# Kernel tuning notes

Measured on AMD Instinct MI355X. Metric: run time of the kernel, lower is better.

The kernel has to match this reference:

```python
import jax, jax.numpy as jnp
import numpy as np

R, K, H_IN, W_IN = 512, 17, 56, 56   # rois, keypoints, heatmap size
ROI_H = ROI_W = 96                   # = ceil(BOX_LEN), fixed by construction
BOX_LEN = 95.5                       # all boxes have this side length
A = -0.75                            # PyTorch bicubic coefficient


def _cubic(x):
    x = jnp.abs(x)
    near = ((A + 2.0) * x - (A + 3.0)) * x * x + 1.0
    far = A * (((x - 5.0) * x + 8.0) * x - 4.0)
    return jnp.where(x <= 1.0, near, jnp.where(x < 2.0, far, 0.0))


def _resize_matrix(out_size, in_size):
    """Dense [out,in] bicubic interpolation matrix (align_corners=False, border-replicate)."""
    scale = in_size / out_size
    src = (jnp.arange(out_size, dtype=jnp.float32) + 0.5) * scale - 0.5
    base = jnp.floor(src).astype(jnp.int32)
    taps = base[:, None] + jnp.arange(-1, 3)                      # [out, 4]
    w = _cubic(src[:, None] - taps.astype(jnp.float32))           # weights from unclamped dist
    taps = jnp.clip(taps, 0, in_size - 1)                         # replicate border
    rows = jnp.broadcast_to(jnp.arange(out_size)[:, None], taps.shape)
    return jnp.zeros((out_size, in_size), jnp.float32).at[rows, taps].add(w)


def setup_inputs() -> dict:
    key = jax.random.key(0)
    k1, k2 = jax.random.split(key)
    masks = jax.random.normal(k1, (R, K, H_IN, W_IN), dtype=jnp.float32)
    offs = jax.random.uniform(k2, (R, 2), jnp.float32, 0.0, 400.0)
    # corner format (c0_start, c1_start, c0_end, c1_end); all lengths == BOX_LEN
    boxes = jnp.concatenate([offs, offs + BOX_LEN], axis=1)
    return {"masks": masks, "boxes": boxes}


def reference(masks, boxes):
    My = _resize_matrix(ROI_H, H_IN)   # [ROI_H, H_IN]
    Mx = _resize_matrix(ROI_W, W_IN)   # [ROI_W, W_IN]
    # separable bicubic resize of every ROI heatmap: [R,K,ROI_H,ROI_W]
    roi = jnp.einsum('hi,rkij,wj->rkhw', My, masks, Mx)
    flat = roi.reshape(R, K, ROI_H * ROI_W)
    pos = jnp.argmax(flat, axis=-1)                                # [R,K]
    y = pos // ROI_W
    x = pos % ROI_W
    scores = jnp.take_along_axis(flat, pos[..., None], axis=-1)[..., 0]  # logit at argmax
    len0 = jnp.maximum(boxes[:, 2] - boxes[:, 0], 1.0)
    len1 = jnp.maximum(boxes[:, 3] - boxes[:, 1], 1.0)
    corr0 = (len0 / ROI_H)[:, None]
    corr1 = (len1 / ROI_W)[:, None]
    p0 = (y.astype(jnp.float32) + 0.5) * corr0 + boxes[:, 0:1]
    p1 = (x.astype(jnp.float32) + 0.5) * corr1 + boxes[:, 1:2]
    predictions = jnp.stack([p0, p1, jnp.ones_like(p0)], axis=1)   # [R, n_dim+1, K]
    return predictions, scores
```

## Files before the change

### kernel.cpp

```cpp
#include <hip/hip_runtime.h>

#define R_    512
#define K_    17
#define HIN   56
#define WIN   56
#define OUTS  96
#define NMAP  (R_ * K_)
#define NT    384
#define RST   98
#define TROWS 60

typedef float v2f __attribute__((ext_vector_type(2)));

constexpr float cubic_c(float xin) {
    float x = xin < 0.0f ? -xin : xin;
    const float A = -0.75f;
    if (x <= 1.0f) return ((A + 2.0f) * x - (A + 3.0f)) * x * x + 1.0f;
    if (x < 2.0f)  return A * (((x - 5.0f) * x + 8.0f) * x - 4.0f);
    return 0.0f;
}

struct XTabT {
    float w[OUTS][4];
    int   s[OUTS];
    constexpr XTabT() : w{}, s{} {
        for (int o = 0; o < OUTS; ++o) {
            float src = ((float)o + 0.5f) * (56.0f / 96.0f) - 0.5f;
            int base = (int)src;
            if ((float)base > src) --base;
            int st = base - 1;
            if (st < 0) st = 0;
            if (st > HIN - 4) st = HIN - 4;
            s[o] = st;
            for (int q = 0; q < 4; ++q) {
                int tap = base - 1 + q;
                float wt = cubic_c(src - (float)tap);
                int p = tap < 0 ? 0 : (tap > HIN - 1 ? HIN - 1 : tap);
                w[o][p - st] += wt;
            }
        }
    }
};
constexpr XTabT XT;

struct YTabT {
    float w[12][4];
    int   d[12];
    constexpr YTabT() : w{}, d{} {
        for (int ph = 0; ph < 12; ++ph) {
            float src = ((float)ph + 0.5f) * (56.0f / 96.0f) - 0.5f;
            int base = (int)src;
            if ((float)base > src) --base;
            d[ph] = base - 1;
            for (int q = 0; q < 4; ++q)
                w[ph][q] = cubic_c(src - (float)(base - 1 + q));
        }
    }
};
constexpr YTabT YT;

template<int G>
__device__ __forceinline__ void p1_cols(const float* __restrict__ r0,
                                        const float* __restrict__ r1,
                                        v2f* __restrict__ dst) {
    constexpr int FS = (G == 0) ? 0 : (G == 1) ? 2 : (G == 2) ? 4
                     : (G == 3) ? 6 : (G == 4) ? 9 : 11;
    constexpr int NF = (G == 2 || G == 3) ? 4 : 3;
    v2f rr[NF * 4];
    const float4* A = (const float4*)r0 + FS;
    const float4* B = (const float4*)r1 + FS;
#pragma unroll
    for (int i = 0; i < NF; ++i) {
        float4 a = A[i], b = B[i];
        rr[4 * i + 0] = (v2f){a.x, b.x};
        rr[4 * i + 1] = (v2f){a.y, b.y};
        rr[4 * i + 2] = (v2f){a.z, b.z};
        rr[4 * i + 3] = (v2f){a.w, b.w};
    }
#pragma unroll
    for (int i = 0; i < 8; ++i) {
        const int o0 = 16 * G + 2 * i, o1 = o0 + 1;
        const int s0 = XT.s[o0] - 4 * FS, s1 = XT.s[o1] - 4 * FS;
        v2f a0 = rr[s0] * (v2f){XT.w[o0][0], XT.w[o0][0]};
        a0 = __builtin_elementwise_fma((v2f){XT.w[o0][1], XT.w[o0][1]}, rr[s0 + 1], a0);
        a0 = __builtin_elementwise_fma((v2f){XT.w[o0][2], XT.w[o0][2]}, rr[s0 + 2], a0);
        a0 = __builtin_elementwise_fma((v2f){XT.w[o0][3], XT.w[o0][3]}, rr[s0 + 3], a0);
        v2f a1 = rr[s1] * (v2f){XT.w[o1][0], XT.w[o1][0]};
        a1 = __builtin_elementwise_fma((v2f){XT.w[o1][1], XT.w[o1][1]}, rr[s1 + 1], a1);
        a1 = __builtin_elementwise_fma((v2f){XT.w[o1][2], XT.w[o1][2]}, rr[s1 + 2], a1);
        a1 = __builtin_elementwise_fma((v2f){XT.w[o1][3], XT.w[o1][3]}, rr[s1 + 3], a1);
        float4 st = {a0.x, a0.y, a1.x, a1.y};
        *(float4*)(dst + 2 * i) = st;
    }
}

__device__ __forceinline__ v2f yv(const v2f* __restrict__ c, int hh) {
    const int ph = hh % 12, bb = hh / 12;
    const int i0 = 7 * bb + YT.d[ph] + 2;
    v2f acc = c[i0] * (v2f){YT.w[ph][0], YT.w[ph][0]};
    acc = __builtin_elementwise_fma((v2f){YT.w[ph][1], YT.w[ph][1]}, c[i0 + 1], acc);
    acc = __builtin_elementwise_fma((v2f){YT.w[ph][2], YT.w[ph][2]}, c[i0 + 2], acc);
    acc = __builtin_elementwise_fma((v2f){YT.w[ph][3], YT.w[ph][3]}, c[i0 + 3], acc);
    return acc;
}

__global__ __launch_bounds__(NT)
void _Keypointer_kernel(const float* __restrict__ masks,
                        const float* __restrict__ boxes,
                        float* __restrict__ out) {
    __shared__ __align__(16) v2f tmp[TROWS * RST];
    __shared__ v2f wmax[6];
    __shared__ int candp[2];

    const int t   = threadIdx.x;
    const int bm0 = 2 * blockIdx.x;
    const int g   = t >> 6;
    const int w   = t & 63;

    const int srcrow = min(max(w - 2, 0), HIN - 1);
    const int phys   = min(w, TROWS - 1);
    const float* r0 = masks + (size_t)bm0 * (HIN * WIN) + srcrow * WIN;
    const float* r1 = r0 + HIN * WIN;
    v2f* dst = tmp + phys * RST + 16 * g;
    if      (g == 0) p1_cols<0>(r0, r1, dst);
    else if (g == 1) p1_cols<1>(r0, r1, dst);
    else if (g == 2) p1_cols<2>(r0, r1, dst);
    else if (g == 3) p1_cols<3>(r0, r1, dst);
    else if (g == 4) p1_cols<4>(r0, r1, dst);
    else             p1_cols<5>(r0, r1, dst);

    if (t == 0) { candp[0] = 0x7fffffff; candp[1] = 0x7fffffff; }
    __syncthreads();

    const int q    = t / 96;
    const int col  = t - 96 * q;
    const int h0   = 24 * q;
    const v2f* cb  = tmp + (14 * q) * RST + col;
    v2f c[18];
#pragma unroll
    for (int i = 0; i < 18; ++i) c[i] = cb[i * RST];

    v2f vmax = {-INFINITY, -INFINITY};
#pragma unroll
    for (int hh = 0; hh < 24; ++hh)
        vmax = __builtin_elementwise_max(vmax, yv(c, hh));

    float m0 = vmax.x, m1 = vmax.y;
#pragma unroll
    for (int off = 32; off > 0; off >>= 1) {
        m0 = fmaxf(m0, __shfl_down(m0, off, 64));
        m1 = fmaxf(m1, __shfl_down(m1, off, 64));
    }
    if (w == 0) wmax[g] = (v2f){m0, m1};
    __syncthreads();

    const float M0 = fmaxf(fmaxf(fmaxf(wmax[0].x, wmax[1].x), fmaxf(wmax[2].x, wmax[3].x)),
                           fmaxf(wmax[4].x, wmax[5].x));
    const float M1 = fmaxf(fmaxf(fmaxf(wmax[0].y, wmax[1].y), fmaxf(wmax[2].y, wmax[3].y)),
                           fmaxf(wmax[4].y, wmax[5].y));

    if (vmax.x == M0 || vmax.y == M1) {
        int c0 = 0x7fffffff, c1 = 0x7fffffff;
#pragma unroll
        for (int hh = 0; hh < 24; ++hh) {
            v2f a = yv(c, hh);
            int fp = (h0 + hh) * OUTS + col;
            if (a.x == M0) c0 = min(c0, fp);
            if (a.y == M1) c1 = min(c1, fp);
        }
        if (c0 != 0x7fffffff) atomicMin(&candp[0], c0);
        if (c1 != 0x7fffffff) atomicMin(&candp[1], c1);
    }
    __syncthreads();

    if (t < 2) {
        const int map = bm0 + t;
        const float M = t ? M1 : M0;
        const int bp  = candp[t];
        const int r = map / K_, k = map - r * K_;
        const int y = bp / OUTS, x = bp - y * OUTS;
        const float b0f = boxes[r * 4 + 0], b1f = boxes[r * 4 + 1];
        const float b2f = boxes[r * 4 + 2], b3f = boxes[r * 4 + 3];
        const float corr0 = fmaxf(b2f - b0f, 1.0f) / (float)OUTS;
        const float corr1 = fmaxf(b3f - b1f, 1.0f) / (float)OUTS;
        const float p0 = ((float)y + 0.5f) * corr0 + b0f;
        const float p1 = ((float)x + 0.5f) * corr1 + b1f;
        out[(r * 3 + 0) * K_ + k] = p0;
        out[(r * 3 + 1) * K_ + k] = p1;
        out[(r * 3 + 2) * K_ + k] = 1.0f;
        out[R_ * 3 * K_ + r * K_ + k] = M;
    }
}

extern "C" void kernel_launch(void* const* d_in, const int* in_sizes, int n_in,
                              void* d_out, int out_size, void* d_ws, size_t ws_size,
                              hipStream_t stream) {
    const float* masks = (const float*)d_in[0];
    const float* boxes = (const float*)d_in[1];
    float* out = (float*)d_out;
    _Keypointer_kernel<<<NMAP / 2, NT, 0, stream>>>(masks, boxes, out);
}
```

Measured before the change: 159.3 us.

## Make kernel persistent with register prefetch of next map pair

Launches a fixed grid where each block processes several map pairs in a loop. It prefetches the next pair's mask rows into registers while computing the current pair's horizontal pass and reduction. This is meant to hide global load latency and reduce per-block launch overhead, at the cost of extra registers and an additional barrier per iteration.

After: 242.1 us. +51.9%, slower.

```diff
diff --git a/kernel.cpp b/kernel.cpp
--- a/kernel.cpp
+++ b/kernel.cpp
@@ -7,6 +7,8 @@
 #define OUTS  96
 #define NMAP  (R_ * K_)
 #define NT    384
+#define GRID  1088
+#define ITERS 4
 #define RST   98
 #define TROWS 60
 
@@ -59,23 +61,35 @@
 };
 constexpr YTabT YT;
 
+template<int G> struct P1G {
+    static constexpr int FS = (G == 0) ? 0 : (G == 1) ? 2 : (G == 2) ? 4
+                            : (G == 3) ? 6 : (G == 4) ? 9 : 11;
+    static constexpr int NF = (G == 2 || G == 3) ? 4 : 3;
+};
+
 template<int G>
-__device__ __forceinline__ void p1_cols(const float* __restrict__ r0,
+__device__ __forceinline__ void p1_load(const float* __restrict__ r0,
                                         const float* __restrict__ r1,
+                                        float4* __restrict__ pa,
+                                        float4* __restrict__ pb) {
+    const float4* A = (const float4*)r0 + P1G<G>::FS;
+    const float4* B = (const float4*)r1 + P1G<G>::FS;
+#pragma unroll
+    for (int i = 0; i < P1G<G>::NF; ++i) { pa[i] = A[i]; pb[i] = B[i]; }
+}
+
+template<int G>
+__device__ __forceinline__ void p1_comp(const float4* __restrict__ pa,
+                                        const float4* __restrict__ pb,
                                         v2f* __restrict__ dst) {
-    constexpr int FS = (G == 0) ? 0 : (G == 1) ? 2 : (G == 2) ? 4
-                     : (G == 3) ? 6 : (G == 4) ? 9 : 11;
-    constexpr int NF = (G == 2 || G == 3) ? 4 : 3;
+    constexpr int FS = P1G<G>::FS, NF = P1G<G>::NF;
     v2f rr[NF * 4];
-    const float4* A = (const float4*)r0 + FS;
-    const float4* B = (const float4*)r1 + FS;
 #pragma unroll
     for (int i = 0; i < NF; ++i) {
-        float4 a = A[i], b = B[i];
-        rr[4 * i + 0] = (v2f){a.x, b.x};
-        rr[4 * i + 1] = (v2f){a.y, b.y};
-        rr[4 * i + 2] = (v2f){a.z, b.z};
-        rr[4 * i + 3] = (v2f){a.w, b.w};
+        rr[4 * i + 0] = (v2f){pa[i].x, pb[i].x};
+        rr[4 * i + 1] = (v2f){pa[i].y, pb[i].y};
+        rr[4 * i + 2] = (v2f){pa[i].z, pb[i].z};
+        rr[4 * i + 3] = (v2f){pa[i].w, pb[i].w};
     }
 #pragma unroll
     for (int i = 0; i < 8; ++i) {
@@ -94,6 +108,25 @@
     }
 }
 
+__device__ __forceinline__ void do_load(int g, const float* r0, const float* r1,
+                                        float4* pa, float4* pb) {
+    if      (g == 0) p1_load<0>(r0, r1, pa, pb);
+    else if (g == 1) p1_load<1>(r0, r1, pa, pb);
+    else if (g == 2) p1_load<2>(r0, r1, pa, pb);
+    else if (g == 3) p1_load<3>(r0, r1, pa, pb);
+    else if (g == 4) p1_load<4>(r0, r1, pa, pb);
+    else             p1_load<5>(r0, r1, pa, pb);
+}
+
+__device__ __forceinline__ void do_comp(int g, const float4* pa, const float4* pb, v2f* dst) {
+    if      (g == 0) p1_comp<0>(pa, pb, dst);
+    else if (g == 1) p1_comp<1>(pa, pb, dst);
+    else if (g == 2) p1_comp<2>(pa, pb, dst);
+    else if (g == 3) p1_comp<3>(pa, pb, dst);
+    else if (g == 4) p1_comp<4>(pa, pb, dst);
+    else             p1_comp<5>(pa, pb, dst);
+}
+
 __device__ __forceinline__ v2f yv(const v2f* __restrict__ c, int hh) {
     const int ph = hh % 12, bb = hh / 12;
     const int i0 = 7 * bb + YT.d[ph] + 2;
@@ -113,82 +146,95 @@
     __shared__ int candp[2];
 
     const int t   = threadIdx.x;
-    const int bm0 = 2 * blockIdx.x;
     const int g   = t >> 6;
     const int w   = t & 63;
 
     const int srcrow = min(max(w - 2, 0), HIN - 1);
     const int phys   = min(w, TROWS - 1);
-    const float* r0 = masks + (size_t)bm0 * (HIN * WIN) + srcrow * WIN;
-    const float* r1 = r0 + HIN * WIN;
     v2f* dst = tmp + phys * RST + 16 * g;
-    if      (g == 0) p1_cols<0>(r0, r1, dst);
-    else if (g == 1) p1_cols<1>(r0, r1, dst);
-    else if (g == 2) p1_cols<2>(r0, r1, dst);
-    else if (g == 3) p1_cols<3>(r0, r1, dst);
-    else if (g == 4) p1_cols<4>(r0, r1, dst);
-    else             p1_cols<5>(r0, r1, dst);
-
-    if (t == 0) { candp[0] = 0x7fffffff; candp[1] = 0x7fffffff; }
-    __syncthreads();
-
-    const int q    = t / 96;
-    const int col  = t - 96 * q;
-    const int h0   = 24 * q;
-    const v2f* cb  = tmp + (14 * q) * RST + col;
-    v2f c[18];
-#pragma unroll
-    for (int i = 0; i < 18; ++i) c[i] = cb[i * RST];
-
-    v2f vmax = {-INFINITY, -INFINITY};
-#pragma unroll
-    for (int hh = 0; hh < 24; ++hh)
-        vmax = __builtin_elementwise_max(vmax, yv(c, hh));
-
-    float m0 = vmax.x, m1 = vmax.y;
-#pragma unroll
-    for (int off = 32; off > 0; off >>= 1) {
-        m0 = fmaxf(m0, __shfl_down(m0, off, 64));
-        m1 = fmaxf(m1, __shfl_down(m1, off, 64));
-    }
-    if (w == 0) wmax[g] = (v2f){m0, m1};
-    __syncthreads();
-
-    const float M0 = fmaxf(fmaxf(fmaxf(wmax[0].x, wmax[1].x), fmaxf(wmax[2].x, wmax[3].x)),
-                           fmaxf(wmax[4].x, wmax[5].x));
-    const float M1 = fmaxf(fmaxf(fmaxf(wmax[0].y, wmax[1].y), fmaxf(wmax[2].y, wmax[3].y)),
-                           fmaxf(wmax[4].y, wmax[5].y));
-
-    if (vmax.x == M0 || vmax.y == M1) {
-        int c0 = 0x7fffffff, c1 = 0x7fffffff;
-#pragma unroll
-        for (int hh = 0; hh < 24; ++hh) {
-            v2f a = yv(c, hh);
-            int fp = (h0 + hh) * OUTS + col;
-            if (a.x == M0) c0 = min(c0, fp);
-            if (a.y == M1) c1 = min(c1, fp);
-        }
-        if (c0 != 0x7fffffff) atomicMin(&candp[0], c0);
-        if (c1 != 0x7fffffff) atomicMin(&candp[1], c1);
-    }
-    __syncthreads();
-
-    if (t < 2) {
-        const int map = bm0 + t;
-        const float M = t ? M1 : M0;
-        const int bp  = candp[t];
-        const int r = map / K_, k = map - r * K_;
-        const int y = bp / OUTS, x = bp - y * OUTS;
-        const float b0f = boxes[r * 4 + 0], b1f = boxes[r * 4 + 1];
-        const float b2f = boxes[r * 4 + 2], b3f = boxes[r * 4 + 3];
-        const float corr0 = fmaxf(b2f - b0f, 1.0f) / (float)OUTS;
-        const float corr1 = fmaxf(b3f - b1f, 1.0f) / (float)OUTS;
-        const float p0 = ((float)y + 0.5f) * corr0 + b0f;
-        const float p1 = ((float)x + 0.5f) * corr1 + b1f;
-        out[(r * 3 + 0) * K_ + k] = p0;
-        out[(r * 3 + 1) * K_ + k] = p1;
-        out[(r * 3 + 2) * K_ + k] = 1.0f;
-        out[R_ * 3 * K_ + r * K_ + k] = M;
+
+    float4 pa[4], pb[4];
+
+    int pair = blockIdx.x;
+    {
+        const float* r0 = masks + (size_t)(2 * pair) * (HIN * WIN) + srcrow * WIN;
+        do_load(g, r0, r0 + HIN * WIN, pa, pb);
+    }
+
+    for (int it = 0; it < ITERS; ++it) {
+        const int bm0 = 2 * pair;
+        const int nxt = pair + GRID;
+
+        if (t == 0) { candp[0] = 0x7fffffff; candp[1] = 0x7fffffff; }
+
+        do_comp(g, pa, pb, dst);
+
+        if (it + 1 < ITERS) {
+            const float* r0 = masks + (size_t)(2 * nxt) * (HIN * WIN) + srcrow * WIN;
+            do_load(g, r0, r0 + HIN * WIN, pa, pb);
+        }
+        __syncthreads();
+
+        const int q    = t / 96;
+        const int col  = t - 96 * q;
+        const int h0   = 24 * q;
+        const v2f* cb  = tmp + (14 * q) * RST + col;
+        v2f c[18];
+#pragma unroll
+        for (int i = 0; i < 18; ++i) c[i] = cb[i * RST];
+
+        v2f vmax = {-INFINITY, -INFINITY};
+#pragma unroll
+        for (int hh = 0; hh < 24; ++hh)
+            vmax = __builtin_elementwise_max(vmax, yv(c, hh));
+
+        float m0 = vmax.x, m1 = vmax.y;
+#pragma unroll
+        for (int off = 32; off > 0; off >>= 1) {
+            m0 = fmaxf(m0, __shfl_down(m0, off, 64));
+            m1 = fmaxf(m1, __shfl_down(m1, off, 64));
+        }
+        if (w == 0) wmax[g] = (v2f){m0, m1};
+        __syncthreads();
+
+        const float M0 = fmaxf(fmaxf(fmaxf(wmax[0].x, wmax[1].x), fmaxf(wmax[2].x, wmax[3].x)),
+                               fmaxf(wmax[4].x, wmax[5].x));
+        const float M1 = fmaxf(fmaxf(fmaxf(wmax[0].y, wmax[1].y), fmaxf(wmax[2].y, wmax[3].y)),
+                               fmaxf(wmax[4].y, wmax[5].y));
+
+        if (vmax.x == M0 || vmax.y == M1) {
+            int c0 = 0x7fffffff, c1 = 0x7fffffff;
+#pragma unroll
+            for (int hh = 0; hh < 24; ++hh) {
+                v2f a = yv(c, hh);
+                int fp = (h0 + hh) * OUTS + col;
+                if (a.x == M0) c0 = min(c0, fp);
+                if (a.y == M1) c1 = min(c1, fp);
+            }
+            if (c0 != 0x7fffffff) atomicMin(&candp[0], c0);
+            if (c1 != 0x7fffffff) atomicMin(&candp[1], c1);
+        }
+        __syncthreads();
+
+        if (t < 2) {
+            const int map = bm0 + t;
+            const float M = t ? M1 : M0;
+            const int bp  = candp[t];
+            const int r = map / K_, k = map - r * K_;
+            const int y = bp / OUTS, x = bp - y * OUTS;
+            const float b0f = boxes[r * 4 + 0], b1f = boxes[r * 4 + 1];
+            const float b2f = boxes[r * 4 + 2], b3f = boxes[r * 4 + 3];
+            const float corr0 = fmaxf(b2f - b0f, 1.0f) / (float)OUTS;
+            const float corr1 = fmaxf(b3f - b1f, 1.0f) / (float)OUTS;
+            const float p0 = ((float)y + 0.5f) * corr0 + b0f;
+            const float p1 = ((float)x + 0.5f) * corr1 + b1f;
+            out[(r * 3 + 0) * K_ + k] = p0;
+            out[(r * 3 + 1) * K_ + k] = p1;
+            out[(r * 3 + 2) * K_ + k] = 1.0f;
+            out[R_ * 3 * K_ + r * K_ + k] = M;
+        }
+        __syncthreads();
+        pair = nxt;
     }
 }
 
@@ -198,5 +244,5 @@
     const float* masks = (const float*)d_in[0];
     const float* boxes = (const float*)d_in[1];
     float* out = (float*)d_out;
-    _Keypointer_kernel<<<NMAP / 2, NT, 0, stream>>>(masks, boxes, out);
-}
+    _Keypointer_kernel<<<GRID, NT, 0, stream>>>(masks, boxes, out);
+}
```

## Process each map pair with one wavefront looping over column strips

Applied to the files above, without the earlier changes.

Each block shrinks from six wavefronts to a single 64-lane wavefront. That wavefront walks the six 16-column strips in sequence, double-buffering the global loads for the next strip while the current one computes, and staging each strip in a small LDS tile. Block-wide __syncthreads and the shared atomicMin candidate search are replaced by LDS waitcnt fences and a shuffle-based argmax that tracks both value and position. This removes cross-wave sync and the second recompute pass, at the cost of more serial work per wave and reliance on in-wave LDS ordering.

Measured after the change: 180.8 us. 1.13x slower.

```diff
diff --git a/kernel.cpp b/kernel.cpp
--- a/kernel.cpp
+++ b/kernel.cpp
@@ -6,11 +6,18 @@
 #define WIN   56
 #define OUTS  96
 #define NMAP  (R_ * K_)
-#define NT    384
-#define RST   98
+#define NT    64
+#define GRID  (NMAP / 2)
+#define WST   18
 #define TROWS 60
 
 typedef float v2f __attribute__((ext_vector_type(2)));
+
+#define LDS_FENCE() do {                                      \
+        __builtin_amdgcn_sched_barrier(0);                    \
+        asm volatile("s_waitcnt lgkmcnt(0)" ::: "memory");    \
+        __builtin_amdgcn_sched_barrier(0);                    \
+    } while (0)
 
 constexpr float cubic_c(float xin) {
     float x = xin < 0.0f ? -xin : xin;
@@ -59,42 +66,12 @@
 };
 constexpr YTabT YT;
 
-template<int G>
-__device__ __forceinline__ void p1_cols(const float* __restrict__ r0,
-                                        const float* __restrict__ r1,
-                                        v2f* __restrict__ dst) {
-    constexpr int FS = (G == 0) ? 0 : (G == 1) ? 2 : (G == 2) ? 4
-                     : (G == 3) ? 6 : (G == 4) ? 9 : 11;
-    constexpr int NF = (G == 2 || G == 3) ? 4 : 3;
-    v2f rr[NF * 4];
-    const float4* A = (const float4*)r0 + FS;
-    const float4* B = (const float4*)r1 + FS;
-#pragma unroll
-    for (int i = 0; i < NF; ++i) {
-        float4 a = A[i], b = B[i];
-        rr[4 * i + 0] = (v2f){a.x, b.x};
-        rr[4 * i + 1] = (v2f){a.y, b.y};
-        rr[4 * i + 2] = (v2f){a.z, b.z};
-        rr[4 * i + 3] = (v2f){a.w, b.w};
-    }
-#pragma unroll
-    for (int i = 0; i < 8; ++i) {
-        const int o0 = 16 * G + 2 * i, o1 = o0 + 1;
-        const int s0 = XT.s[o0] - 4 * FS, s1 = XT.s[o1] - 4 * FS;
-        v2f a0 = rr[s0] * (v2f){XT.w[o0][0], XT.w[o0][0]};
-        a0 = __builtin_elementwise_fma((v2f){XT.w[o0][1], XT.w[o0][1]}, rr[s0 + 1], a0);
-        a0 = __builtin_elementwise_fma((v2f){XT.w[o0][2], XT.w[o0][2]}, rr[s0 + 2], a0);
-        a0 = __builtin_elementwise_fma((v2f){XT.w[o0][3], XT.w[o0][3]}, rr[s0 + 3], a0);
-        v2f a1 = rr[s1] * (v2f){XT.w[o1][0], XT.w[o1][0]};
-        a1 = __builtin_elementwise_fma((v2f){XT.w[o1][1], XT.w[o1][1]}, rr[s1 + 1], a1);
-        a1 = __builtin_elementwise_fma((v2f){XT.w[o1][2], XT.w[o1][2]}, rr[s1 + 2], a1);
-        a1 = __builtin_elementwise_fma((v2f){XT.w[o1][3], XT.w[o1][3]}, rr[s1 + 3], a1);
-        float4 st = {a0.x, a0.y, a1.x, a1.y};
-        *(float4*)(dst + 2 * i) = st;
-    }
-}
-
-__device__ __forceinline__ v2f yv(const v2f* __restrict__ c, int hh) {
+template<int G> struct FSv {
+    static constexpr int v = (G == 0) ? 0 : (G == 1) ? 1 : (G == 2) ? 4
+                           : (G == 3) ? 6 : (G == 4) ? 8 : 10;
+};
+
+__device__ __forceinline__ v2f yv(const v2f* c, int hh) {
     const int ph = hh % 12, bb = hh / 12;
     const int i0 = 7 * bb + YT.d[ph] + 2;
     v2f acc = c[i0] * (v2f){YT.w[ph][0], YT.w[ph][0]};
@@ -104,91 +81,132 @@
     return acc;
 }
 
+template<int G>
+__device__ __forceinline__ void strip_comp(float4 a0, float4 a1, float4 a2, float4 a3,
+                                           float4 b0, float4 b1, float4 b2, float4 b3,
+                                           v2f* wrow,
+                                           const v2f* crd,
+                                           int pbase,
+                                           float& m0, int& p0, float& m1, int& p1) {
+    constexpr int FS = FSv<G>::v;
+    v2f rr[16];
+    rr[0]  = (v2f){a0.x, b0.x}; rr[1]  = (v2f){a0.y, b0.y};
+    rr[2]  = (v2f){a0.z, b0.z}; rr[3]  = (v2f){a0.w, b0.w};
+    rr[4]  = (v2f){a1.x, b1.x}; rr[5]  = (v2f){a1.y, b1.y};
+    rr[6]  = (v2f){a1.z, b1.z}; rr[7]  = (v2f){a1.w, b1.w};
+    rr[8]  = (v2f){a2.x, b2.x}; rr[9]  = (v2f){a2.y, b2.y};
+    rr[10] = (v2f){a2.z, b2.z}; rr[11] = (v2f){a2.w, b2.w};
+    rr[12] = (v2f){a3.x, b3.x}; rr[13] = (v2f){a3.y, b3.y};
+    rr[14] = (v2f){a3.z, b3.z}; rr[15] = (v2f){a3.w, b3.w};
+
+    LDS_FENCE();
+#pragma unroll
+    for (int i = 0; i < 8; ++i) {
+        const int o0 = 16 * G + 2 * i, o1 = o0 + 1;
+        const int s0 = XT.s[o0] - 4 * FS, s1 = XT.s[o1] - 4 * FS;
+        v2f x0 = rr[s0] * (v2f){XT.w[o0][0], XT.w[o0][0]};
+        x0 = __builtin_elementwise_fma((v2f){XT.w[o0][1], XT.w[o0][1]}, rr[s0 + 1], x0);
+        x0 = __builtin_elementwise_fma((v2f){XT.w[o0][2], XT.w[o0][2]}, rr[s0 + 2], x0);
+        x0 = __builtin_elementwise_fma((v2f){XT.w[o0][3], XT.w[o0][3]}, rr[s0 + 3], x0);
+        v2f x1 = rr[s1] * (v2f){XT.w[o1][0], XT.w[o1][0]};
+        x1 = __builtin_elementwise_fma((v2f){XT.w[o1][1], XT.w[o1][1]}, rr[s1 + 1], x1);
+        x1 = __builtin_elementwise_fma((v2f){XT.w[o1][2], XT.w[o1][2]}, rr[s1 + 2], x1);
+        x1 = __builtin_elementwise_fma((v2f){XT.w[o1][3], XT.w[o1][3]}, rr[s1 + 3], x1);
+        float4 st = {x0.x, x0.y, x1.x, x1.y};
+        *(float4*)(wrow + 2 * i) = st;
+    }
+    LDS_FENCE();
+
+    v2f c[18];
+#pragma unroll
+    for (int i = 0; i < 18; ++i) c[i] = crd[i * WST];
+
+    v2f sv = {-INFINITY, -INFINITY};
+    int h0i = 0, h1i = 0;
+#pragma unroll
+    for (int hh = 0; hh < 24; ++hh) {
+        v2f a = yv(c, hh);
+        if (a.x > sv.x) { sv.x = a.x; h0i = hh; }
+        if (a.y > sv.y) { sv.y = a.y; h1i = hh; }
+    }
+    const int fp0 = pbase + 16 * G + h0i * 96;
+    const int fp1 = pbase + 16 * G + h1i * 96;
+    if (sv.x > m0 || (sv.x == m0 && fp0 < p0)) { m0 = sv.x; p0 = fp0; }
+    if (sv.y > m1 || (sv.y == m1 && fp1 < p1)) { m1 = sv.y; p1 = fp1; }
+}
+
 __global__ __launch_bounds__(NT)
 void _Keypointer_kernel(const float* __restrict__ masks,
                         const float* __restrict__ boxes,
                         float* __restrict__ out) {
-    __shared__ __align__(16) v2f tmp[TROWS * RST];
-    __shared__ v2f wmax[6];
-    __shared__ int candp[2];
-
-    const int t   = threadIdx.x;
+    __shared__ __align__(16) v2f tmp[TROWS * WST];
+
+    const int w   = threadIdx.x;
     const int bm0 = 2 * blockIdx.x;
-    const int g   = t >> 6;
-    const int w   = t & 63;
 
     const int srcrow = min(max(w - 2, 0), HIN - 1);
     const int phys   = min(w, TROWS - 1);
     const float* r0 = masks + (size_t)bm0 * (HIN * WIN) + srcrow * WIN;
     const float* r1 = r0 + HIN * WIN;
-    v2f* dst = tmp + phys * RST + 16 * g;
-    if      (g == 0) p1_cols<0>(r0, r1, dst);
-    else if (g == 1) p1_cols<1>(r0, r1, dst);
-    else if (g == 2) p1_cols<2>(r0, r1, dst);
-    else if (g == 3) p1_cols<3>(r0, r1, dst);
-    else if (g == 4) p1_cols<4>(r0, r1, dst);
-    else             p1_cols<5>(r0, r1, dst);
-
-    if (t == 0) { candp[0] = 0x7fffffff; candp[1] = 0x7fffffff; }
-    __syncthreads();
-
-    const int q    = t / 96;
-    const int col  = t - 96 * q;
-    const int h0   = 24 * q;
-    const v2f* cb  = tmp + (14 * q) * RST + col;
-    v2f c[18];
-#pragma unroll
-    for (int i = 0; i < 18; ++i) c[i] = cb[i * RST];
-
-    v2f vmax = {-INFINITY, -INFINITY};
-#pragma unroll
-    for (int hh = 0; hh < 24; ++hh)
-        vmax = __builtin_elementwise_max(vmax, yv(c, hh));
-
-    float m0 = vmax.x, m1 = vmax.y;
-#pragma unroll
-    for (int off = 32; off > 0; off >>= 1) {
-        m0 = fmaxf(m0, __shfl_down(m0, off, 64));
-        m1 = fmaxf(m1, __shfl_down(m1, off, 64));
-    }
-    if (w == 0) wmax[g] = (v2f){m0, m1};
-    __syncthreads();
-
-    const float M0 = fmaxf(fmaxf(fmaxf(wmax[0].x, wmax[1].x), fmaxf(wmax[2].x, wmax[3].x)),
-                           fmaxf(wmax[4].x, wmax[5].x));
-    const float M1 = fmaxf(fmaxf(fmaxf(wmax[0].y, wmax[1].y), fmaxf(wmax[2].y, wmax[3].y)),
-                           fmaxf(wmax[4].y, wmax[5].y));
-
-    if (vmax.x == M0 || vmax.y == M1) {
-        int c0 = 0x7fffffff, c1 = 0x7fffffff;
-#pragma unroll
-        for (int hh = 0; hh < 24; ++hh) {
-            v2f a = yv(c, hh);
-            int fp = (h0 + hh) * OUTS + col;
-            if (a.x == M0) c0 = min(c0, fp);
-            if (a.y == M1) c1 = min(c1, fp);
+    v2f* wrow = tmp + phys * WST;
+
+    const int cc = w & 15, q = w >> 4;
+    const v2f* crd = tmp + (14 * q) * WST + cc;
+    const int pbase = (24 * q) * OUTS + cc;
+
+    float m0 = -INFINITY, m1 = -INFINITY;
+    int   p0 = 0x7fffffff, p1 = 0x7fffffff;
+
+    float4 A0, A1, A2, A3, B0, B1, B2, B3;
+    float4 C0, C1, C2, C3, D0, D1, D2, D3;
+
+#define LOADS(FS_, X0, X1, X2, X3, Y0, Y1, Y2, Y3) {            \
+        const float4* _A = (const float4*)r0 + (FS_);           \
+        const float4* _B = (const float4*)r1 + (FS_);           \
+        X0 = _A[0]; X1 = _A[1]; X2 = _A[2]; X3 = _A[3];         \
+        Y0 = _B[0]; Y1 = _B[1]; Y2 = _B[2]; Y3 = _B[3]; }
+
+    LOADS(0,  A0, A1, A2, A3, B0, B1, B2, B3)
+    LOADS(1,  C0, C1, C2, C3, D0, D1, D2, D3)
+    strip_comp<0>(A0, A1, A2, A3, B0, B1, B2, B3, wrow, crd, pbase, m0, p0, m1, p1);
+    LOADS(4,  A0, A1, A2, A3, B0, B1, B2, B3)
+    strip_comp<1>(C0, C1, C2, C3, D0, D1, D2, D3, wrow, crd, pbase, m0, p0, m1, p1);
+    LOADS(6,  C0, C1, C2, C3, D0, D1, D2, D3)
+    strip_comp<2>(A0, A1, A2, A3, B0, B1, B2, B3, wrow, crd, pbase, m0, p0, m1, p1);
+    LOADS(8,  A0, A1, A2, A3, B0, B1, B2, B3)
+    strip_comp<3>(C0, C1, C2, C3, D0, D1, D2, D3, wrow, crd, pbase, m0, p0, m1, p1);
+    LOADS(10, C0, C1, C2, C3, D0, D1, D2, D3)
+    strip_comp<4>(A0, A1, A2, A3, B0, B1, B2, B3, wrow, crd, pbase, m0, p0, m1, p1);
+    strip_comp<5>(C0, C1, C2, C3, D0, D1, D2, D3, wrow, crd, pbase, m0, p0, m1, p1);
+#undef LOADS
+
+#pragma unroll
+    for (int off = 32; off; off >>= 1) {
+        float t0 = __shfl_xor(m0, off, 64); int u0 = __shfl_xor(p0, off, 64);
+        if (t0 > m0 || (t0 == m0 && u0 < p0)) { m0 = t0; p0 = u0; }
+        float t1 = __shfl_xor(m1, off, 64); int u1 = __shfl_xor(p1, off, 64);
+        if (t1 > m1 || (t1 == m1 && u1 < p1)) { m1 = t1; p1 = u1; }
+    }
+
+    if (w == 0) {
+#pragma unroll
+        for (int mi = 0; mi < 2; ++mi) {
+            const int map = bm0 + mi;
+            const float M = mi ? m1 : m0;
+            const int bp  = mi ? p1 : p0;
+            const int r = map / K_, k = map - r * K_;
+            const int y = bp / OUTS, x = bp - y * OUTS;
+            const float b0f = boxes[r * 4 + 0], b1f = boxes[r * 4 + 1];
+            const float b2f = boxes[r * 4 + 2], b3f = boxes[r * 4 + 3];
+            const float corr0 = fmaxf(b2f - b0f, 1.0f) / (float)OUTS;
+            const float corr1 = fmaxf(b3f - b1f, 1.0f) / (float)OUTS;
+            const float pp0 = ((float)y + 0.5f) * corr0 + b0f;
+            const float pp1 = ((float)x + 0.5f) * corr1 + b1f;
+            out[(r * 3 + 0) * K_ + k] = pp0;
+            out[(r * 3 + 1) * K_ + k] = pp1;
+            out[(r * 3 + 2) * K_ + k] = 1.0f;
+            out[R_ * 3 * K_ + r * K_ + k] = M;
         }
-        if (c0 != 0x7fffffff) atomicMin(&candp[0], c0);
-        if (c1 != 0x7fffffff) atomicMin(&candp[1], c1);
-    }
-    __syncthreads();
-
-    if (t < 2) {
-        const int map = bm0 + t;
-        const float M = t ? M1 : M0;
-        const int bp  = candp[t];
-        const int r = map / K_, k = map - r * K_;
-        const int y = bp / OUTS, x = bp - y * OUTS;
-        const float b0f = boxes[r * 4 + 0], b1f = boxes[r * 4 + 1];
-        const float b2f = boxes[r * 4 + 2], b3f = boxes[r * 4 + 3];
-        const float corr0 = fmaxf(b2f - b0f, 1.0f) / (float)OUTS;
-        const float corr1 = fmaxf(b3f - b1f, 1.0f) / (float)OUTS;
-        const float p0 = ((float)y + 0.5f) * corr0 + b0f;
-        const float p1 = ((float)x + 0.5f) * corr1 + b1f;
-        out[(r * 3 + 0) * K_ + k] = p0;
-        out[(r * 3 + 1) * K_ + k] = p1;
-        out[(r * 3 + 2) * K_ + k] = 1.0f;
-        out[R_ * 3 * K_ + r * K_ + k] = M;
     }
 }
 
@@ -198,5 +216,5 @@
     const float* masks = (const float*)d_in[0];
     const float* boxes = (const float*)d_in[1];
     float* out = (float*)d_out;
-    _Keypointer_kernel<<<NMAP / 2, NT, 0, stream>>>(masks, boxes, out);
-}
+    _Keypointer_kernel<<<GRID, NT, 0, stream>>>(masks, boxes, out);
+}
```
